# Optimization experiments

Measured on AMD Instinct MI355X. Metric: run time of the kernel, lower is better.

Reference implementation:

```python
import jax, jax.numpy as jnp
import numpy as np

T, IN, H, L, OUT = 131072, 60, 14, 3, 7


def setup_inputs() -> dict:
    key = jax.random.key(0)
    ks = jax.random.split(key, 18)
    s = 1.0 / np.sqrt(H)  # torch default LSTM/Linear init scale
    u = lambda k, shp: jax.random.uniform(k, shp, jnp.float32, -s, s)
    return {
        "x": jax.random.normal(ks[0], (T, IN), jnp.float32),
        "h0": jax.random.uniform(ks[1], (L, H), jnp.float32),
        "c0": jax.random.uniform(ks[2], (L, H), jnp.float32),
        "W_ih0": u(ks[3], (4 * H, IN)), "W_hh0": u(ks[4], (4 * H, H)),
        "b_ih0": u(ks[5], (4 * H,)), "b_hh0": u(ks[6], (4 * H,)),
        "W_ih1": u(ks[7], (4 * H, H)), "W_hh1": u(ks[8], (4 * H, H)),
        "b_ih1": u(ks[9], (4 * H,)), "b_hh1": u(ks[10], (4 * H,)),
        "W_ih2": u(ks[11], (4 * H, H)), "W_hh2": u(ks[12], (4 * H, H)),
        "b_ih2": u(ks[13], (4 * H,)), "b_hh2": u(ks[14], (4 * H,)),
        "W_lin": u(ks[15], (OUT, H)), "b_lin": u(ks[16], (OUT,)),
    }


def _cell(xp, h, c, Whh, bhh):
    # PyTorch gate order: i, f, g, o
    g = xp + h @ Whh.T + bhh  # [4H]
    i, f, gg, o = jnp.split(g, 4, axis=-1)
    c = jax.nn.sigmoid(f) * c + jax.nn.sigmoid(i) * jnp.tanh(gg)
    h = jax.nn.sigmoid(o) * jnp.tanh(c)
    return h, c


def reference(x, h0, c0, W_ih0, W_hh0, b_ih0, b_hh0,
              W_ih1, W_hh1, b_ih1, b_hh1,
              W_ih2, W_hh2, b_ih2, b_hh2, W_lin, b_lin):
    # precompute layer-0 input projection (only GEMM that parallelizes over T)
    xw0 = x @ W_ih0.T + b_ih0  # [T, 4H]

    def step(carry, xp):
        h, c = carry  # [L, H] each
        h0n, c0n = _cell(xp, h[0], c[0], W_hh0, b_hh0)
        h1n, c1n = _cell(h0n @ W_ih1.T + b_ih1, h[1], c[1], W_hh1, b_hh1)
        h2n, c2n = _cell(h1n @ W_ih2.T + b_ih2, h[2], c[2], W_hh2, b_hh2)
        return (jnp.stack([h0n, h1n, h2n]), jnp.stack([c0n, c1n, c2n])), h2n

    _, out = jax.lax.scan(step, (h0, c0), xw0)  # out: [T, H]
    return jax.nn.relu(jax.nn.relu(out) @ W_lin.T + b_lin)  # [T, OUT]
```

## Files before the change

### kernel.cpp

```cpp
#include <hip/hip_runtime.h>

#define T_TOT 131072
#define IN_DIM 60
#define H_DIM 14
#define G4 56
#define OUT_DIM 7
#define S_CHUNK 64
#define N_CHUNK (T_TOT / S_CHUNK)
#define WARM 34
#define LOG2E 1.44269504088896340736f
#define LSTRIDE 65
#define SSTRIDE (S_CHUNK * LSTRIDE)

__device__ __forceinline__ float frcp(float x)  { return __builtin_amdgcn_rcpf(x); }
__device__ __forceinline__ float fexp2(float x) { return __builtin_amdgcn_exp2f(x); }
__device__ __forceinline__ float rlane(float v, int l) {
    return __int_as_float(__builtin_amdgcn_readlane(__float_as_int(v), l));
}
template<int CTRL>
__device__ __forceinline__ float qb(float v) {
#if __has_builtin(__builtin_amdgcn_update_dpp)
    return __int_as_float(__builtin_amdgcn_update_dpp(
        0, __float_as_int(v), CTRL, 0xF, 0xF, true));
#else
    return __int_as_float(__builtin_amdgcn_mov_dpp(
        __float_as_int(v), CTRL, 0xF, 0xF, true));
#endif
}

__global__ __launch_bounds__(64)
void prep(const float* __restrict__ Wih0, const float* __restrict__ bih0,
          const float* __restrict__ bhh0, float* __restrict__ WT)
{
    const int i = threadIdx.x;
    for (int idx = i; idx < IN_DIM * G4; idx += 64) {
        const int k = idx / G4, j = idx % G4;
        const float sc = (j >= 28 && j < 42) ? -2.f * LOG2E : -LOG2E;
        WT[idx] = Wih0[j * IN_DIM + k] * sc;
    }
    if (i < G4) {
        const float sc = (i >= 28 && i < 42) ? -2.f * LOG2E : -LOG2E;
        WT[IN_DIM * G4 + i] = (bih0[i] + bhh0[i]) * sc;
    }
}

__global__ __attribute__((amdgpu_flat_work_group_size(256, 256), amdgpu_waves_per_eu(2, 2)))
void xproj(const float* __restrict__ x, const float* __restrict__ WT,
           float* __restrict__ xw0)
{
    const int t = blockIdx.x * 256 + threadIdx.x;
    float xr[IN_DIM];
    const float4* xrow = (const float4*)(x + (size_t)t * IN_DIM);
#pragma unroll
    for (int i = 0; i < IN_DIM / 4; ++i) {
        const float4 v = xrow[i];
        xr[4 * i] = v.x; xr[4 * i + 1] = v.y; xr[4 * i + 2] = v.z; xr[4 * i + 3] = v.w;
    }
    float acc[G4];
#pragma unroll
    for (int j = 0; j < G4; ++j) acc[j] = WT[IN_DIM * G4 + j];
#pragma unroll 2
    for (int k = 0; k < IN_DIM; ++k) {
        const float xk = xr[k];
#pragma unroll
        for (int j = 0; j < G4; ++j) acc[j] = fmaf(xk, WT[k * G4 + j], acc[j]);
    }
    float4* orow = (float4*)(xw0 + (size_t)t * G4);
#pragma unroll
    for (int q = 0; q < G4 / 4; ++q)
        orow[q] = (float4){acc[q], acc[14 + q], acc[28 + q], acc[42 + q]};
}

__global__ __attribute__((amdgpu_flat_work_group_size(64, 64), amdgpu_waves_per_eu(2, 2)))
void lstm_fused(const float* __restrict__ xw0,
                const float* __restrict__ Whh0,
                const float* __restrict__ Wih1, const float* __restrict__ Whh1,
                const float* __restrict__ Wih2, const float* __restrict__ Whh2,
                const float* __restrict__ bih1, const float* __restrict__ bhh1,
                const float* __restrict__ bih2, const float* __restrict__ bhh2,
                const float* __restrict__ h0in, const float* __restrict__ c0in,
                const float* __restrict__ Wlin, const float* __restrict__ blin,
                float* __restrict__ out)
{
    __shared__ float stash[SSTRIDE];

    const int lane = threadIdx.x;
    const int gt = lane & 3;
    const int kq = lane >> 2;
    const int kc = kq > 13 ? 13 : kq;
    const int j  = gt * H_DIM + kc;
    const float sc = (gt == 2) ? -2.f * LOG2E : -LOG2E;

    float w0[H_DIM], wi1[H_DIM], wh1[H_DIM], wi2[H_DIM], wh2[H_DIM];
#pragma unroll
    for (int k = 0; k < H_DIM; ++k) {
        w0[k]  = Whh0[j * H_DIM + k] * sc;
        wi1[k] = Wih1[j * H_DIM + k] * sc;
        wh1[k] = Whh1[j * H_DIM + k] * sc;
        wi2[k] = Wih2[j * H_DIM + k] * sc;
        wh2[k] = Whh2[j * H_DIM + k] * sc;
    }
    const float bias1 = (bih1[j] + bhh1[j]) * sc;
    const float bias2 = (bih2[j] + bhh2[j]) * sc;

    const float amul = (gt == 2) ?  2.f : 1.f;
    const float aadd = (gt == 2) ? -1.f : 0.f;

    const int scol = kq + 16 * gt;
    const int xcol = lane < G4 ? lane : lane - 8;

    const int t0 = blockIdx.x * S_CHUNK;
    float h0v, c0v, h1v, c1v, h2v, c2v;
    int saddr = scol;

    auto gates = [&](float xv, float& a0, float& a1, float& a2) {
        float g0a = xv,    g0b = 0.f;
        float g1a = bias1, g1b = 0.f, g1c = 0.f, g1d = 0.f;
        float g2a = bias2, g2b = 0.f, g2c = 0.f, g2d = 0.f;
#pragma unroll
        for (int k = 0; k < 7; ++k) {
            const float s0a = rlane(h0v, 4 * k), s0b = rlane(h0v, 4 * k + 28);
            const float s1a = rlane(h1v, 4 * k), s1b = rlane(h1v, 4 * k + 28);
            const float s2a = rlane(h2v, 4 * k), s2b = rlane(h2v, 4 * k + 28);
            g0a = fmaf(s0a, w0[k],      g0a);
            g0b = fmaf(s0b, w0[k + 7],  g0b);
            g1a = fmaf(s0a, wi1[k],     g1a);
            g1b = fmaf(s0b, wi1[k + 7], g1b);
            g1c = fmaf(s1a, wh1[k],     g1c);
            g1d = fmaf(s1b, wh1[k + 7], g1d);
            g2a = fmaf(s1a, wi2[k],     g2a);
            g2b = fmaf(s1b, wi2[k + 7], g2b);
            g2c = fmaf(s2a, wh2[k],     g2c);
            g2d = fmaf(s2b, wh2[k + 7], g2d);
        }
        a0 = fmaf(amul, frcp(1.f + fexp2(g0a + g0b)), aadd);
        a1 = fmaf(amul, frcp(1.f + fexp2((g1a + g1b) + (g1c + g1d))), aadd);
        a2 = fmaf(amul, frcp(1.f + fexp2((g2a + g2b) + (g2c + g2d))), aadd);
    };
    auto cellupd = [&](float a, float& cv) -> float {
        const float iv = qb<0x00>(a);
        const float fv = qb<0x55>(a);
        const float gv = qb<0xAA>(a);
        const float ov = qb<0xFF>(a);
        const float cn = fmaf(fv, cv, iv * gv);
        const float th = fmaf(2.f, frcp(1.f + fexp2(-2.f * LOG2E * cn)), -1.f);
        cv = cn;
        return ov * th;
    };
    auto step = [&](float xv, bool store_en) {
        float a0, a1, a2;
        gates(xv, a0, a1, a2);
        h0v = cellupd(a0, c0v);
        h1v = cellupd(a1, c1v);
        h2v = cellupd(a2, c2v);
        if (store_en) { stash[saddr] = h2v; saddr += LSTRIDE; }
    };

    if (blockIdx.x == 0) {
        h0v = h0in[kc]; h1v = h0in[H_DIM + kc]; h2v = h0in[2 * H_DIM + kc];
        c0v = c0in[kc]; c1v = c0in[H_DIM + kc]; c2v = c0in[2 * H_DIM + kc];
        const float* xp = xw0 + xcol;
        float xv = xp[0], xn1 = xp[G4];
        {
            float a0, a1, a2; gates(xv, a0, a1, a2);
            h0v = cellupd(a0, c0v);
            xv = xn1; xn1 = xp[2 * G4]; xp += G4;
        }
        {
            float a0, a1, a2; gates(xv, a0, a1, a2);
            h0v = cellupd(a0, c0v);
            h1v = cellupd(a1, c1v);
            xv = xn1; xn1 = xp[2 * G4]; xp += G4;
        }
#pragma unroll 1
        for (int m = 0; m < S_CHUNK; ++m) {
            step(xv, true);
            xv = xn1; xn1 = xp[2 * G4]; xp += G4;
        }
    } else {
        h0v = h1v = h2v = 0.f; c0v = c1v = c2v = 0.f;
        const float* xp = xw0 + (size_t)(t0 - WARM) * G4 + xcol;
        float x0 = xp[0], x1 = xp[G4], x2 = xp[2 * G4], x3 = xp[3 * G4];
        xp += 4 * G4;
#pragma unroll 1
        for (int m = 0; m < (WARM + 2) / 4; ++m) {
            step(x0, false); x0 = xp[0];
            step(x1, false); x1 = xp[G4];
            step(x2, false); x2 = xp[2 * G4];
            step(x3, false); x3 = xp[3 * G4];
            xp += 4 * G4;
        }
#pragma unroll 1
        for (int m = 0; m < S_CHUNK / 4; ++m) {
            step(x0, true); x0 = xp[0];
            step(x1, true); x1 = xp[G4];
            step(x2, true); x2 = xp[2 * G4];
            step(x3, true); x3 = xp[3 * G4];
            xp += 4 * G4;
        }
    }

    __syncthreads();
    float h[H_DIM];
#pragma unroll
    for (int k = 0; k < H_DIM; ++k) {
        const float v = stash[lane * LSTRIDE + k];
        h[k] = v > 0.f ? v : 0.f;
    }
    float* orow = out + (size_t)(t0 + lane) * OUT_DIM;
#pragma unroll
    for (int o = 0; o < OUT_DIM; ++o) {
        float acc = blin[o];
#pragma unroll
        for (int k = 0; k < H_DIM; ++k) acc = fmaf(h[k], Wlin[o * H_DIM + k], acc);
        orow[o] = acc > 0.f ? acc : 0.f;
    }
}

extern "C" void kernel_launch(void* const* d_in, const int* in_sizes, int n_in,
                              void* d_out, int out_size, void* d_ws, size_t ws_size,
                              hipStream_t stream)
{
    const float* x     = (const float*)d_in[0];
    const float* h0    = (const float*)d_in[1];
    const float* c0    = (const float*)d_in[2];
    const float* W_ih0 = (const float*)d_in[3];
    const float* W_hh0 = (const float*)d_in[4];
    const float* b_ih0 = (const float*)d_in[5];
    const float* b_hh0 = (const float*)d_in[6];
    const float* W_ih1 = (const float*)d_in[7];
    const float* W_hh1 = (const float*)d_in[8];
    const float* b_ih1 = (const float*)d_in[9];
    const float* b_hh1 = (const float*)d_in[10];
    const float* W_ih2 = (const float*)d_in[11];
    const float* W_hh2 = (const float*)d_in[12];
    const float* b_ih2 = (const float*)d_in[13];
    const float* b_hh2 = (const float*)d_in[14];
    const float* W_lin = (const float*)d_in[15];
    const float* b_lin = (const float*)d_in[16];
    float* out = (float*)d_out;

    float* xw0 = (float*)d_ws;
    float* WT  = xw0 + (size_t)(T_TOT + 8) * G4;

    prep<<<1, 64, 0, stream>>>(W_ih0, b_ih0, b_hh0, WT);
    xproj<<<T_TOT / 256, 256, 0, stream>>>(x, WT, xw0);
    lstm_fused<<<N_CHUNK, 64, 0, stream>>>(xw0, W_hh0, W_ih1, W_hh1, W_ih2, W_hh2,
                                           b_ih1, b_hh1, b_ih2, b_hh2, h0, c0,
                                           W_lin, b_lin, out);
}
```

Measured before the change: 214.7 us.

## Broadcast hidden state via LDS and use packed FP32 FMAs for gate dot products

The per-step hidden-state broadcast switches from 42 readlane instructions to each lane writing its h values into a small shared buffer, which every lane then reads back as float2 pairs. The 14-wide gate dot products for all three layers are rewritten with inline-asm v_pk_fma/v_pk_mul/v_pk_add on float2 pairs, roughly halving the FMA instruction count. The trade-off is an LDS write-then-read round trip added to the serial recurrence's critical path. This latency could offset the savings from fewer VALU and scalar ops.

```diff
diff --git a/kernel.cpp b/kernel.cpp
--- a/kernel.cpp
+++ b/kernel.cpp
@@ -12,11 +12,24 @@
 #define LSTRIDE 65
 #define SSTRIDE (S_CHUNK * LSTRIDE)
 
+typedef float v2f __attribute__((ext_vector_type(2)));
+
 __device__ __forceinline__ float frcp(float x)  { return __builtin_amdgcn_rcpf(x); }
 __device__ __forceinline__ float fexp2(float x) { return __builtin_amdgcn_exp2f(x); }
-__device__ __forceinline__ float rlane(float v, int l) {
-    return __int_as_float(__builtin_amdgcn_readlane(__float_as_int(v), l));
-}
+
+__device__ __forceinline__ v2f pkfma(v2f a, v2f b, v2f c) {
+    v2f d; asm("v_pk_fma_f32 %0, %1, %2, %3" : "=v"(d) : "v"(a), "v"(b), "v"(c));
+    return d;
+}
+__device__ __forceinline__ v2f pkmul(v2f a, v2f b) {
+    v2f d; asm("v_pk_mul_f32 %0, %1, %2" : "=v"(d) : "v"(a), "v"(b));
+    return d;
+}
+__device__ __forceinline__ v2f pkadd(v2f a, v2f b) {
+    v2f d; asm("v_pk_add_f32 %0, %1, %2" : "=v"(d) : "v"(a), "v"(b));
+    return d;
+}
+
 template<int CTRL>
 __device__ __forceinline__ float qb(float v) {
 #if __has_builtin(__builtin_amdgcn_update_dpp)
@@ -83,6 +96,7 @@
                 float* __restrict__ out)
 {
     __shared__ float stash[SSTRIDE];
+    __shared__ __align__(16) float hbuf[3 * 64];
 
     const int lane = threadIdx.x;
     const int gt = lane & 3;
@@ -91,51 +105,80 @@
     const int j  = gt * H_DIM + kc;
     const float sc = (gt == 2) ? -2.f * LOG2E : -LOG2E;
 
-    float w0[H_DIM], wi1[H_DIM], wh1[H_DIM], wi2[H_DIM], wh2[H_DIM];
-#pragma unroll
-    for (int k = 0; k < H_DIM; ++k) {
-        w0[k]  = Whh0[j * H_DIM + k] * sc;
-        wi1[k] = Wih1[j * H_DIM + k] * sc;
-        wh1[k] = Whh1[j * H_DIM + k] * sc;
-        wi2[k] = Wih2[j * H_DIM + k] * sc;
-        wh2[k] = Whh2[j * H_DIM + k] * sc;
-    }
-    const float bias1 = (bih1[j] + bhh1[j]) * sc;
-    const float bias2 = (bih2[j] + bhh2[j]) * sc;
+    v2f wp0[7], wpi1[7], wph1[7], wpi2[7], wph2[7];
+#pragma unroll
+    for (int q = 0; q < 7; ++q) {
+        wp0[q]  = v2f{Whh0[j * H_DIM + 2 * q] * sc, Whh0[j * H_DIM + 2 * q + 1] * sc};
+        wpi1[q] = v2f{Wih1[j * H_DIM + 2 * q] * sc, Wih1[j * H_DIM + 2 * q + 1] * sc};
+        wph1[q] = v2f{Whh1[j * H_DIM + 2 * q] * sc, Whh1[j * H_DIM + 2 * q + 1] * sc};
+        wpi2[q] = v2f{Wih2[j * H_DIM + 2 * q] * sc, Wih2[j * H_DIM + 2 * q + 1] * sc};
+        wph2[q] = v2f{Whh2[j * H_DIM + 2 * q] * sc, Whh2[j * H_DIM + 2 * q + 1] * sc};
+    }
+    const v2f bias1v = v2f{(bih1[j] + bhh1[j]) * sc, 0.f};
+    const v2f bias2v = v2f{(bih2[j] + bhh2[j]) * sc, 0.f};
 
     const float amul = (gt == 2) ?  2.f : 1.f;
     const float aadd = (gt == 2) ? -1.f : 0.f;
 
-    const int scol = kq + 16 * gt;
+    const int hoff = kq + 16 * gt;
+    float* hput = hbuf + hoff;
+    const int scol = hoff;
     const int xcol = lane < G4 ? lane : lane - 8;
 
     const int t0 = blockIdx.x * S_CHUNK;
     float h0v, c0v, h1v, c1v, h2v, c2v;
     int saddr = scol;
 
+    const v2f* hb0 = (const v2f*)(hbuf);
+    const v2f* hb1 = (const v2f*)(hbuf + 64);
+    const v2f* hb2 = (const v2f*)(hbuf + 128);
+
     auto gates = [&](float xv, float& a0, float& a1, float& a2) {
-        float g0a = xv,    g0b = 0.f;
-        float g1a = bias1, g1b = 0.f, g1c = 0.f, g1d = 0.f;
-        float g2a = bias2, g2b = 0.f, g2c = 0.f, g2d = 0.f;
-#pragma unroll
-        for (int k = 0; k < 7; ++k) {
-            const float s0a = rlane(h0v, 4 * k), s0b = rlane(h0v, 4 * k + 28);
-            const float s1a = rlane(h1v, 4 * k), s1b = rlane(h1v, 4 * k + 28);
-            const float s2a = rlane(h2v, 4 * k), s2b = rlane(h2v, 4 * k + 28);
-            g0a = fmaf(s0a, w0[k],      g0a);
-            g0b = fmaf(s0b, w0[k + 7],  g0b);
-            g1a = fmaf(s0a, wi1[k],     g1a);
-            g1b = fmaf(s0b, wi1[k + 7], g1b);
-            g1c = fmaf(s1a, wh1[k],     g1c);
-            g1d = fmaf(s1b, wh1[k + 7], g1d);
-            g2a = fmaf(s1a, wi2[k],     g2a);
-            g2b = fmaf(s1b, wi2[k + 7], g2b);
-            g2c = fmaf(s2a, wh2[k],     g2c);
-            g2d = fmaf(s2b, wh2[k + 7], g2d);
-        }
-        a0 = fmaf(amul, frcp(1.f + fexp2(g0a + g0b)), aadd);
-        a1 = fmaf(amul, frcp(1.f + fexp2((g1a + g1b) + (g1c + g1d))), aadd);
-        a2 = fmaf(amul, frcp(1.f + fexp2((g2a + g2b) + (g2c + g2d))), aadd);
+        v2f hp0[7], hp1[7], hp2[7];
+#pragma unroll
+        for (int q = 0; q < 7; ++q) { hp0[q] = hb0[q]; hp1[q] = hb1[q]; hp2[q] = hb2[q]; }
+        v2f A = pkmul(wp0[0], hp0[0]);
+        A = pkfma(wp0[1], hp0[1], A);
+        A = pkfma(wp0[2], hp0[2], A);
+        A = pkfma(wp0[3], hp0[3], A);
+        v2f B = pkmul(wp0[4], hp0[4]);
+        B = pkfma(wp0[5], hp0[5], B);
+        B = pkfma(wp0[6], hp0[6], B);
+        const v2f S0 = pkadd(A, B);
+        v2f IA = pkfma(wpi1[0], hp0[0], bias1v);
+        IA = pkfma(wpi1[1], hp0[1], IA);
+        IA = pkfma(wpi1[2], hp0[2], IA);
+        IA = pkfma(wpi1[3], hp0[3], IA);
+        v2f IB = pkmul(wpi1[4], hp0[4]);
+        IB = pkfma(wpi1[5], hp0[5], IB);
+        IB = pkfma(wpi1[6], hp0[6], IB);
+        v2f HA = pkmul(wph1[0], hp1[0]);
+        HA = pkfma(wph1[1], hp1[1], HA);
+        HA = pkfma(wph1[2], hp1[2], HA);
+        HA = pkfma(wph1[3], hp1[3], HA);
+        v2f HB = pkmul(wph1[4], hp1[4]);
+        HB = pkfma(wph1[5], hp1[5], HB);
+        HB = pkfma(wph1[6], hp1[6], HB);
+        const v2f S1 = pkadd(pkadd(IA, IB), pkadd(HA, HB));
+        v2f JA = pkfma(wpi2[0], hp1[0], bias2v);
+        JA = pkfma(wpi2[1], hp1[1], JA);
+        JA = pkfma(wpi2[2], hp1[2], JA);
+        JA = pkfma(wpi2[3], hp1[3], JA);
+        v2f JB = pkmul(wpi2[4], hp1[4]);
+        JB = pkfma(wpi2[5], hp1[5], JB);
+        JB = pkfma(wpi2[6], hp1[6], JB);
+        v2f KA = pkmul(wph2[0], hp2[0]);
+        KA = pkfma(wph2[1], hp2[1], KA);
+        KA = pkfma(wph2[2], hp2[2], KA);
+        KA = pkfma(wph2[3], hp2[3], KA);
+        v2f KB = pkmul(wph2[4], hp2[4]);
+        KB = pkfma(wph2[5], hp2[5], KB);
+        KB = pkfma(wph2[6], hp2[6], KB);
+        const v2f S2 = pkadd(pkadd(JA, JB), pkadd(KA, KB));
+
+        a0 = fmaf(amul, frcp(1.f + fexp2((S0.x + S0.y) + xv)), aadd);
+        a1 = fmaf(amul, frcp(1.f + fexp2(S1.x + S1.y)), aadd);
+        a2 = fmaf(amul, frcp(1.f + fexp2(S2.x + S2.y)), aadd);
     };
     auto cellupd = [&](float a, float& cv) -> float {
         const float iv = qb<0x00>(a);
@@ -153,23 +196,27 @@
         h0v = cellupd(a0, c0v);
         h1v = cellupd(a1, c1v);
         h2v = cellupd(a2, c2v);
+        hput[0] = h0v; hput[64] = h1v; hput[128] = h2v;
         if (store_en) { stash[saddr] = h2v; saddr += LSTRIDE; }
     };
 
     if (blockIdx.x == 0) {
         h0v = h0in[kc]; h1v = h0in[H_DIM + kc]; h2v = h0in[2 * H_DIM + kc];
         c0v = c0in[kc]; c1v = c0in[H_DIM + kc]; c2v = c0in[2 * H_DIM + kc];
+        hput[0] = h0v; hput[64] = h1v; hput[128] = h2v;
         const float* xp = xw0 + xcol;
         float xv = xp[0], xn1 = xp[G4];
         {
             float a0, a1, a2; gates(xv, a0, a1, a2);
             h0v = cellupd(a0, c0v);
+            hput[0] = h0v;
             xv = xn1; xn1 = xp[2 * G4]; xp += G4;
         }
         {
             float a0, a1, a2; gates(xv, a0, a1, a2);
             h0v = cellupd(a0, c0v);
             h1v = cellupd(a1, c1v);
+            hput[0] = h0v; hput[64] = h1v;
             xv = xn1; xn1 = xp[2 * G4]; xp += G4;
         }
 #pragma unroll 1
@@ -179,6 +226,7 @@
         }
     } else {
         h0v = h1v = h2v = 0.f; c0v = c1v = c2v = 0.f;
+        hput[0] = 0.f; hput[64] = 0.f; hput[128] = 0.f;
         const float* xp = xw0 + (size_t)(t0 - WARM) * G4 + xcol;
         float x0 = xp[0], x1 = xp[G4], x2 = xp[2 * G4], x3 = xp[3 * G4];
         xp += 4 * G4;
```

Result: no change. 211.9 us (-1.3%).
